# Optimization experiments

Measured on AMD Instinct MI355X. Metric: run time of the kernel, lower is better.

## Reference

```python
import jax, jax.numpy as jnp
import numpy as np

N, E = 65536, 524288
IN_DIM, HID_DIM, OUT_DIM = 1024, 512, 256


def setup_inputs() -> dict:
    key = jax.random.key(0)
    k1, k2, k3, k4, k5, k6 = jax.random.split(key, 6)
    h = jax.random.normal(k1, (N, IN_DIM), dtype=jnp.float32)
    src = jax.random.randint(k2, (E,), 0, N, dtype=jnp.int64)
    dst = jax.random.randint(k3, (E,), 0, N, dtype=jnp.int64)
    # Glorot-uniform weights as in DGL GraphConv
    lim1 = float(np.sqrt(6.0 / (IN_DIM + HID_DIM)))
    lim2 = float(np.sqrt(6.0 / (HID_DIM + OUT_DIM)))
    W1 = jax.random.uniform(k4, (IN_DIM, HID_DIM), jnp.float32, -lim1, lim1)
    W2 = jax.random.uniform(k5, (HID_DIM, OUT_DIM), jnp.float32, -lim2, lim2)
    b1 = jnp.zeros((HID_DIM,), jnp.float32)
    b2 = jnp.zeros((OUT_DIM,), jnp.float32)
    return {"h": h, "W1": W1, "b1": b1, "W2": W2, "b2": b2, "src": src, "dst": dst}


def _graph_conv(x, W, b, src, dst, inv_sqrt_dout, inv_sqrt_din):
    # DGL GraphConv, norm='both': D_in^{-1/2} A D_out^{-1/2} X W + b
    # Apply dense transform first (in_dim >= out_dim path in DGL) -- same math.
    x = x * inv_sqrt_dout[:, None]
    x = x @ W  # [N, out]
    agg = jax.ops.segment_sum(x[src], dst, num_segments=x.shape[0])  # scatter-add over edges
    return agg * inv_sqrt_din[:, None] + b


def reference(h, W1, b1, W2, b2, src, dst):
    n = h.shape[0]
    ones = jnp.ones((src.shape[0],), h.dtype)
    deg_out = jnp.maximum(jax.ops.segment_sum(ones, src, num_segments=n), 1.0)
    deg_in = jnp.maximum(jax.ops.segment_sum(ones, dst, num_segments=n), 1.0)
    inv_sqrt_dout = jax.lax.rsqrt(deg_out)
    inv_sqrt_din = jax.lax.rsqrt(deg_in)
    x = _graph_conv(h, W1, b1, src, dst, inv_sqrt_dout, inv_sqrt_din)
    x = jax.nn.elu(x)  # act; dropout p=0 -> identity
    out = _graph_conv(x, W2, b2, src, dst, inv_sqrt_dout, inv_sqrt_din)
    return out  # last_act = Identity
```

## Files before the change

### kernel.cpp

```cpp
#include <hip/hip_runtime.h>
#include <hip/hip_bf16.h>

#define IN_DIM 1024
#define HID 512
#define OUTD 256

typedef __attribute__((ext_vector_type(8))) short short8;
typedef __attribute__((ext_vector_type(4))) float f32x4;
typedef __attribute__((ext_vector_type(8))) unsigned short ushort8e;
typedef __attribute__((ext_vector_type(4))) unsigned short ushort4e;
typedef __attribute__((ext_vector_type(4))) unsigned int uint4e;

template<int F> struct VecSel;
template<> struct VecSel<8> { using T = ushort8e; };
template<> struct VecSel<4> { using T = ushort4e; };


__device__ inline unsigned short f2bf(float f) {
    union { float f; unsigned u; } v; v.f = f;
    unsigned r = (v.u + 0x7FFF + ((v.u >> 16) & 1)) >> 16;
    return (unsigned short)r;
}

__device__ inline float bf2f(unsigned short u) {
    union { unsigned u; float f; } v; v.u = ((unsigned)u) << 16; return v.f;
}

__device__ inline unsigned pkbf(float a, float b) {
    __hip_bfloat162 h = __float22bfloat162_rn(float2{a, b});
    union { __hip_bfloat162 h; unsigned u; } v; v.h = h; return v.u;
}

__device__ inline void gload16(const void* g, void* l) {
    __builtin_amdgcn_global_load_lds(
        (const __attribute__((address_space(1))) void*)g,
        (__attribute__((address_space(3))) void*)l, 16, 0, 0);
}


__global__ void deg_kernel(const int* __restrict__ src, const int* __restrict__ dst,
                           int* __restrict__ dego, int* __restrict__ degi, int E) {
    int i = blockIdx.x * blockDim.x + threadIdx.x;
    if (i < E) {
        atomicAdd(&dego[src[i]], 1);
        atomicAdd(&degi[dst[i]], 1);
    }
}

__global__ void invsqrt_kernel(const int* __restrict__ dego, const int* __restrict__ degi,
                               float* __restrict__ iso, float* __restrict__ isi, int n) {
    int i = blockIdx.x * blockDim.x + threadIdx.x;
    if (i < n) {
        iso[i] = rsqrtf(fmaxf((float)dego[i], 1.0f));
        isi[i] = rsqrtf(fmaxf((float)degi[i], 1.0f));
    }
}


__global__ __launch_bounds__(256) void scan_block(const int* __restrict__ deg,
                                                  int* __restrict__ excl,
                                                  int* __restrict__ partials) {
    __shared__ int tmp[256];
    int tid = threadIdx.x;
    int i = blockIdx.x * 256 + tid;
    int v = deg[i];
    tmp[tid] = v;
    __syncthreads();
    #pragma unroll
    for (int off = 1; off < 256; off <<= 1) {
        int t = (tid >= off) ? tmp[tid - off] : 0;
        __syncthreads();
        tmp[tid] += t;
        __syncthreads();
    }
    excl[i] = tmp[tid] - v;
    if (tid == 255) partials[blockIdx.x] = tmp[255];
}

__global__ __launch_bounds__(256) void scan_partials(int* __restrict__ partials) {
    __shared__ int tmp[256];
    int tid = threadIdx.x;
    int v = partials[tid];
    tmp[tid] = v;
    __syncthreads();
    #pragma unroll
    for (int off = 1; off < 256; off <<= 1) {
        int t = (tid >= off) ? tmp[tid - off] : 0;
        __syncthreads();
        tmp[tid] += t;
        __syncthreads();
    }
    partials[tid] = tmp[tid] - v;
}

__global__ __launch_bounds__(256) void scan_add(const int* __restrict__ excl,
                                                const int* __restrict__ partials,
                                                const int* __restrict__ deg,
                                                int* __restrict__ row_start,
                                                int* __restrict__ cursor, int n) {
    int i = blockIdx.x * 256 + threadIdx.x;
    int v = excl[i] + partials[blockIdx.x];
    row_start[i] = v;
    cursor[i] = v;
    if (i == n - 1) row_start[n] = v + deg[i];
}

__global__ void csr_fill(const int* __restrict__ src, const int* __restrict__ dst,
                         int* __restrict__ cursor, int* __restrict__ eidx, int E) {
    int e = blockIdx.x * blockDim.x + threadIdx.x;
    if (e < E) {
        int pos = atomicAdd(&cursor[dst[e]], 1);
        eidx[pos] = src[e];
    }
}


__global__ void transpose_cvt(const float* __restrict__ W, unsigned short* __restrict__ Wt,
                              int K, int N) {
    int i = blockIdx.x * 256 + threadIdx.x;
    if (i < N * K) {
        int n = i / K, k = i - n * K;
        Wt[i] = f2bf(W[(size_t)k * N + n]);
    }
}


#define TM 128
#define TN 128
#define TK 64
#define NXCD 8

template<int AF32>
__global__ __launch_bounds__(256) void gemm_bf16_mfma(
    const void* __restrict__ Ap, const unsigned short* __restrict__ Bt,
    unsigned short* __restrict__ Cb, int M, int K, int Nc)
{
    __shared__ unsigned short As[2][TM][TK];
    __shared__ unsigned short Bs[2][TN][TK];

    const int tid  = threadIdx.x;
    const int lane = tid & 63;
    const int wave = tid >> 6;
    const int wr = wave >> 1, wc = wave & 1;
    const int lrow = lane & 15;
    const int lkg  = lane >> 4;

    const int nwg = gridDim.x;
    const int per = nwg / NXCD;
    const int lin = blockIdx.x;
    const int newlin = (lin % NXCD) * per + lin / NXCD;
    const int ncb = Nc / TN;
    const int m0 = (newlin / ncb) * TM;
    const int n0 = (newlin % ncb) * TN;

    int srow[4], sq[4];
    #pragma unroll
    for (int i = 0; i < 4; ++i) {
        int s = i * 256 + wave * 64 + lane;
        srow[i] = s >> 3;
        sq[i] = (s & 7) ^ ((s >> 3) & 7);
    }

    char* AsB = (char*)&As[0][0][0];
    char* BsB = (char*)&Bs[0][0][0];

    const float* Af = (const float*)Ap;
    const unsigned short* Ab = (const unsigned short*)Ap;

    auto stageOp = [&](const unsigned short* G, int rc0, int kt, char* opBase, int buf) {
        const int k0 = kt * TK;
        #pragma unroll
        for (int i = 0; i < 4; ++i)
            gload16(G + (size_t)(rc0 + srow[i]) * K + k0 + sq[i] * 8,
                    opBase + buf * 16384 + (i * 256 + wave * 64) * 16);
    };

    const int rA = tid >> 2;
    const int g  = tid & 3;
    const int qp0 = (2 * g) ^ (rA & 7);
    const int qp1 = (2 * g + 1) ^ (rA & 7);
    float4 L[8];
    auto loadA = [&](int kt) {
        const float* p0 = Af + (size_t)(m0 + rA) * K + kt * TK + g * 16;
        const float* p1 = p0 + (size_t)64 * K;
        L[0] = *reinterpret_cast<const float4*>(p0);
        L[1] = *reinterpret_cast<const float4*>(p0 + 4);
        L[2] = *reinterpret_cast<const float4*>(p0 + 8);
        L[3] = *reinterpret_cast<const float4*>(p0 + 12);
        L[4] = *reinterpret_cast<const float4*>(p1);
        L[5] = *reinterpret_cast<const float4*>(p1 + 4);
        L[6] = *reinterpret_cast<const float4*>(p1 + 8);
        L[7] = *reinterpret_cast<const float4*>(p1 + 12);
    };
    auto writeA = [&](int buf) {
        #pragma unroll
        for (int r = 0; r < 2; ++r) {
            const float4 f0 = L[r * 4 + 0], f1 = L[r * 4 + 1];
            const float4 f2 = L[r * 4 + 2], f3 = L[r * 4 + 3];
            uint4e a, b;
            a[0] = pkbf(f0.x, f0.y); a[1] = pkbf(f0.z, f0.w);
            a[2] = pkbf(f1.x, f1.y); a[3] = pkbf(f1.z, f1.w);
            b[0] = pkbf(f2.x, f2.y); b[1] = pkbf(f2.z, f2.w);
            b[2] = pkbf(f3.x, f3.y); b[3] = pkbf(f3.z, f3.w);
            char* rowb = AsB + buf * 16384 + (rA + r * 64) * 128;
            *reinterpret_cast<uint4e*>(rowb + qp0 * 16) = a;
            *reinterpret_cast<uint4e*>(rowb + qp1 * 16) = b;
        }
    };

    f32x4 acc[4][4] = {};

    stageOp(Bt, n0, 0, BsB, 0);
    if (AF32) { loadA(0); writeA(0); }
    else       stageOp(Ab, m0, 0, AsB, 0);
    __syncthreads();

    const int nk = K / TK;
    for (int kt = 0; kt < nk; ++kt) {
        const int cur = kt & 1, nxt = cur ^ 1;

        if (kt + 1 < nk) {
            stageOp(Bt, n0, kt + 1, BsB, nxt);
            if (AF32) loadA(kt + 1);
            else      stageOp(Ab, m0, kt + 1, AsB, nxt);
        }

        #pragma unroll
        for (int ks = 0; ks < 2; ++ks) {
            short8 af[4], bfr[4];
            #pragma unroll
            for (int mi = 0; mi < 4; ++mi) {
                const int row = wr * 64 + mi * 16 + lrow;
                const int qp = (ks * 4 + lkg) ^ (lrow & 7);
                af[mi] = *reinterpret_cast<const short8*>(&As[cur][row][qp * 8]);
            }
            #pragma unroll
            for (int ni = 0; ni < 4; ++ni) {
                const int row = wc * 64 + ni * 16 + lrow;
                const int qp = (ks * 4 + lkg) ^ (lrow & 7);
                bfr[ni] = *reinterpret_cast<const short8*>(&Bs[cur][row][qp * 8]);
            }
            #pragma unroll
            for (int mi = 0; mi < 4; ++mi)
                #pragma unroll
                for (int ni = 0; ni < 4; ++ni)
                    acc[mi][ni] = __builtin_amdgcn_mfma_f32_16x16x32_bf16(
                        af[mi], bfr[ni], acc[mi][ni], 0, 0, 0);
        }

        if (AF32 && kt + 1 < nk) writeA(nxt);

        __syncthreads();
    }

    #pragma unroll
    for (int mi = 0; mi < 4; ++mi)
        #pragma unroll
        for (int ni = 0; ni < 4; ++ni)
            #pragma unroll
            for (int r = 0; r < 4; ++r)
                Cb[(size_t)(m0 + wr * 64 + mi * 16 + lkg * 4 + r) * Nc
                   + (n0 + wc * 64 + ni * 16 + lrow)] = f2bf(acc[mi][ni][r]);
}


template<int DIM, bool LAYER1>
__global__ __launch_bounds__(256) void aggregate(
    const int* __restrict__ row_start, const int* __restrict__ eidx,
    const unsigned short* __restrict__ Xb, const float* __restrict__ isi,
    const float* __restrict__ iso, const float* __restrict__ bias,
    unsigned short* __restrict__ out_bf, float* __restrict__ out_f)
{
    constexpr int F = DIM / 64;
    using VecT = typename VecSel<F>::T;
    const int node = blockIdx.x * 4 + (threadIdx.x >> 6);
    const int lane = threadIdx.x & 63;

    const int beg = row_start[node];
    const int end = row_start[node + 1];
    const unsigned short* base = Xb + lane * F;

    float acc[F] = {};
    int e = beg;
    for (; e + 3 < end; e += 4) {
        int i0 = eidx[e], i1 = eidx[e + 1], i2 = eidx[e + 2], i3 = eidx[e + 3];
        float s0 = 1.f, s1 = 1.f, s2 = 1.f, s3 = 1.f;
        if (LAYER1) { s0 = iso[i0]; s1 = iso[i1]; s2 = iso[i2]; s3 = iso[i3]; }
        VecT v0 = *reinterpret_cast<const VecT*>(base + (size_t)i0 * DIM);
        VecT v1 = *reinterpret_cast<const VecT*>(base + (size_t)i1 * DIM);
        VecT v2 = *reinterpret_cast<const VecT*>(base + (size_t)i2 * DIM);
        VecT v3 = *reinterpret_cast<const VecT*>(base + (size_t)i3 * DIM);
        #pragma unroll
        for (int f = 0; f < F; ++f) {
            if (LAYER1) {
                acc[f] = fmaf(s0, bf2f(v0[f]), acc[f]);
                acc[f] = fmaf(s1, bf2f(v1[f]), acc[f]);
                acc[f] = fmaf(s2, bf2f(v2[f]), acc[f]);
                acc[f] = fmaf(s3, bf2f(v3[f]), acc[f]);
            } else {
                acc[f] += bf2f(v0[f]); acc[f] += bf2f(v1[f]);
                acc[f] += bf2f(v2[f]); acc[f] += bf2f(v3[f]);
            }
        }
    }
    for (; e < end; ++e) {
        int i0 = eidx[e];
        float s0 = LAYER1 ? iso[i0] : 1.f;
        VecT v0 = *reinterpret_cast<const VecT*>(base + (size_t)i0 * DIM);
        #pragma unroll
        for (int f = 0; f < F; ++f)
            acc[f] = LAYER1 ? fmaf(s0, bf2f(v0[f]), acc[f]) : acc[f] + bf2f(v0[f]);
    }

    const float si = isi[node];
    float bv[F];
    #pragma unroll
    for (int q = 0; q < F / 4; ++q)
        *reinterpret_cast<float4*>(&bv[q * 4]) =
            *reinterpret_cast<const float4*>(bias + lane * F + q * 4);

    if (LAYER1) {
        const float so = iso[node];
        short8 o;
        #pragma unroll
        for (int f = 0; f < F; ++f) {
            float v = acc[f] * si + bv[f];
            v = v > 0.f ? v : expm1f(v);
            o[f] = (short)f2bf(v * so);
        }
        *reinterpret_cast<short8*>(out_bf + (size_t)node * DIM + lane * F) = o;
    } else {
        #pragma unroll
        for (int q = 0; q < F / 4; ++q) {
            float4 v = make_float4(acc[q * 4 + 0] * si + bv[q * 4 + 0],
                                   acc[q * 4 + 1] * si + bv[q * 4 + 1],
                                   acc[q * 4 + 2] * si + bv[q * 4 + 2],
                                   acc[q * 4 + 3] * si + bv[q * 4 + 3]);
            *reinterpret_cast<float4*>(out_f + (size_t)node * DIM + lane * F + q * 4) = v;
        }
    }
}


extern "C" void kernel_launch(void* const* d_in, const int* in_sizes, int n_in,
                              void* d_out, int out_size, void* d_ws, size_t ws_size,
                              hipStream_t stream) {
    const float* h  = (const float*)d_in[0];
    const float* W1 = (const float*)d_in[1];
    const float* b1 = (const float*)d_in[2];
    const float* W2 = (const float*)d_in[3];
    const float* b2 = (const float*)d_in[4];
    const int*   src = (const int*)d_in[5];
    const int*   dst = (const int*)d_in[6];

    const int N = in_sizes[0] / IN_DIM;
    const int E = in_sizes[5];
    float* out = (float*)d_out;

    int* dego      = (int*)d_ws;
    int* degi      = dego + N;
    int* excl      = degi + N;
    int* partials  = excl + N;
    int* row_start = partials + 256;
    int* cursor    = row_start + N + 64;
    int* eidx      = cursor + N;
    float* iso     = (float*)(eidx + E);
    float* isi     = iso + N;
    unsigned short* W1t = (unsigned short*)(isi + N);
    unsigned short* W2t = W1t + (size_t)IN_DIM * HID;
    unsigned short* X1b = W2t + (size_t)HID * OUTD;
    unsigned short* X2b = X1b;
    unsigned short* R2h = X1b + (size_t)N * HID;

    hipMemsetAsync(dego, 0, sizeof(int) * (size_t)2 * N, stream);

    deg_kernel<<<(E + 255) / 256, 256, 0, stream>>>(src, dst, dego, degi, E);
    invsqrt_kernel<<<(N + 255) / 256, 256, 0, stream>>>(dego, degi, iso, isi, N);

    scan_block<<<N / 256, 256, 0, stream>>>(degi, excl, partials);
    scan_partials<<<1, 256, 0, stream>>>(partials);
    scan_add<<<N / 256, 256, 0, stream>>>(excl, partials, degi, row_start, cursor, N);
    csr_fill<<<(E + 255) / 256, 256, 0, stream>>>(src, dst, cursor, eidx, E);

    transpose_cvt<<<(IN_DIM * HID + 255) / 256, 256, 0, stream>>>(W1, W1t, IN_DIM, HID);
    transpose_cvt<<<(HID * OUTD + 255) / 256, 256, 0, stream>>>(W2, W2t, HID, OUTD);

    gemm_bf16_mfma<1><<<(N / TM) * (HID / TN), 256, 0, stream>>>(
        h, W1t, X1b, N, IN_DIM, HID);
    aggregate<HID, true><<<N / 4, 256, 0, stream>>>(
        row_start, eidx, X1b, isi, iso, b1, R2h, nullptr);

    gemm_bf16_mfma<0><<<(N / TM) * (OUTD / TN), 256, 0, stream>>>(
        R2h, W2t, X2b, N, HID, OUTD);
    aggregate<OUTD, false><<<N / 4, 256, 0, stream>>>(
        row_start, eidx, X2b, isi, iso, b2, nullptr, out);
}
```

Measured before the change: 431.7 us.

## Use full-width 64x512 GEMM1 tile with fused out-degree row scaling

Replaces the layer-1 GEMM with a kernel where each block computes a 64-row by full 512-column tile, so the fp32 input matrix is read and converted to bf16 only once instead of once per column tile. The out-degree normalization is folded into the A-load conversion, which removes the per-edge iso gather and FMA from the layer-1 aggregation. The new kernel uses a single LDS buffer with two barriers per K step and no prefetch overlap, and its 128 accumulator tiles per wave raise register pressure. Scaling before the bf16 rounding also shifts where rounding error enters.

Result: slower. 462.9 us (+7.2%).

```diff
diff --git a/kernel.cpp b/kernel.cpp
--- a/kernel.cpp
+++ b/kernel.cpp
@@ -9,7 +9,6 @@
 typedef __attribute__((ext_vector_type(4))) float f32x4;
 typedef __attribute__((ext_vector_type(8))) unsigned short ushort8e;
 typedef __attribute__((ext_vector_type(4))) unsigned short ushort4e;
-typedef __attribute__((ext_vector_type(4))) unsigned int uint4e;
 
 template<int F> struct VecSel;
 template<> struct VecSel<8> { using T = ushort8e; };
@@ -24,11 +23,6 @@
 
 __device__ inline float bf2f(unsigned short u) {
     union { unsigned u; float f; } v; v.u = ((unsigned)u) << 16; return v.f;
-}
-
-__device__ inline unsigned pkbf(float a, float b) {
-    __hip_bfloat162 h = __float22bfloat162_rn(float2{a, b});
-    union { __hip_bfloat162 h; unsigned u; } v; v.h = h; return v.u;
 }
 
 __device__ inline void gload16(const void* g, void* l) {
@@ -125,14 +119,96 @@
 }
 
 
+__global__ __launch_bounds__(256) void gemm1_wide(
+    const float* __restrict__ A, const unsigned short* __restrict__ Bt,
+    const float* __restrict__ rowscale, unsigned short* __restrict__ Cb, int M)
+{
+    __shared__ unsigned short As[64][32];
+    __shared__ unsigned short Bs[512][32];
+
+    const int tid  = threadIdx.x;
+    const int lane = tid & 63;
+    const int wave = tid >> 6;
+    const int lrow = lane & 15;
+    const int lkg  = lane >> 4;
+
+    const int m0 = blockIdx.x * 64;
+
+    char* AsB = (char*)&As[0][0];
+    char* BsB = (char*)&Bs[0][0];
+
+    const int rA = tid >> 2;
+    const int g  = tid & 3;
+    const int qpA = g ^ ((rA >> 1) & 3);
+    const float sc = rowscale[m0 + rA];
+
+    const int rslot = (lkg ^ ((lrow >> 1) & 3)) * 8;
+
+    f32x4 acc[4][8] = {};
+
+    const int nk = IN_DIM / 32;
+    for (int kt = 0; kt < nk; ++kt) {
+        const int k0 = kt * 32;
+
+        #pragma unroll
+        for (int i = 0; i < 8; ++i) {
+            const int s = i * 256 + wave * 64 + lane;
+            const int r = s >> 2;
+            const int q = (s & 3) ^ ((s >> 3) & 3);
+            gload16(Bt + (size_t)r * IN_DIM + k0 + q * 8,
+                    BsB + (i * 256 + wave * 64) * 16);
+        }
+
+        {
+            const float* pa = A + (size_t)(m0 + rA) * IN_DIM + k0 + g * 8;
+            float4 x = *reinterpret_cast<const float4*>(pa);
+            float4 y = *reinterpret_cast<const float4*>(pa + 4);
+            short8 kv;
+            kv[0] = (short)f2bf(x.x * sc); kv[1] = (short)f2bf(x.y * sc);
+            kv[2] = (short)f2bf(x.z * sc); kv[3] = (short)f2bf(x.w * sc);
+            kv[4] = (short)f2bf(y.x * sc); kv[5] = (short)f2bf(y.y * sc);
+            kv[6] = (short)f2bf(y.z * sc); kv[7] = (short)f2bf(y.w * sc);
+            *reinterpret_cast<short8*>(AsB + rA * 64 + qpA * 16) = kv;
+        }
+
+        __syncthreads();
+
+        short8 af[4], bfr[8];
+        #pragma unroll
+        for (int mi = 0; mi < 4; ++mi)
+            af[mi] = *reinterpret_cast<const short8*>(&As[mi * 16 + lrow][rslot]);
+        #pragma unroll
+        for (int ni = 0; ni < 8; ++ni)
+            bfr[ni] = *reinterpret_cast<const short8*>(&Bs[wave * 128 + ni * 16 + lrow][rslot]);
+
+        #pragma unroll
+        for (int mi = 0; mi < 4; ++mi)
+            #pragma unroll
+            for (int ni = 0; ni < 8; ++ni)
+                acc[mi][ni] = __builtin_amdgcn_mfma_f32_16x16x32_bf16(
+                    af[mi], bfr[ni], acc[mi][ni], 0, 0, 0);
+
+        __syncthreads();
+    }
+
+    #pragma unroll
+    for (int mi = 0; mi < 4; ++mi)
+        #pragma unroll
+        for (int ni = 0; ni < 8; ++ni)
+            #pragma unroll
+            for (int r = 0; r < 4; ++r)
+                Cb[(size_t)(m0 + mi * 16 + lkg * 4 + r) * HID
+                   + (wave * 128 + ni * 16 + lrow)] = f2bf(acc[mi][ni][r]);
+}
+
+
 #define TM 128
 #define TN 128
 #define TK 64
 #define NXCD 8
 
-template<int AF32>
-__global__ __launch_bounds__(256) void gemm_bf16_mfma(
-    const void* __restrict__ Ap, const unsigned short* __restrict__ Bt,
+__global__ __launch_bounds__(256) void gemm2_bf16(
+    const unsigned short* __restrict__ Ab, const unsigned short* __restrict__ Bt,
     unsigned short* __restrict__ Cb, int M, int K, int Nc)
 {
     __shared__ unsigned short As[2][TM][TK];
@@ -164,9 +240,6 @@
     char* AsB = (char*)&As[0][0][0];
     char* BsB = (char*)&Bs[0][0][0];
 
-    const float* Af = (const float*)Ap;
-    const unsigned short* Ab = (const unsigned short*)Ap;
-
     auto stageOp = [&](const unsigned short* G, int rc0, int kt, char* opBase, int buf) {
         const int k0 = kt * TK;
         #pragma unroll
@@ -175,44 +248,10 @@
                     opBase + buf * 16384 + (i * 256 + wave * 64) * 16);
     };
 
-    const int rA = tid >> 2;
-    const int g  = tid & 3;
-    const int qp0 = (2 * g) ^ (rA & 7);
-    const int qp1 = (2 * g + 1) ^ (rA & 7);
-    float4 L[8];
-    auto loadA = [&](int kt) {
-        const float* p0 = Af + (size_t)(m0 + rA) * K + kt * TK + g * 16;
-        const float* p1 = p0 + (size_t)64 * K;
-        L[0] = *reinterpret_cast<const float4*>(p0);
-        L[1] = *reinterpret_cast<const float4*>(p0 + 4);
-        L[2] = *reinterpret_cast<const float4*>(p0 + 8);
-        L[3] = *reinterpret_cast<const float4*>(p0 + 12);
-        L[4] = *reinterpret_cast<const float4*>(p1);
-        L[5] = *reinterpret_cast<const float4*>(p1 + 4);
-        L[6] = *reinterpret_cast<const float4*>(p1 + 8);
-        L[7] = *reinterpret_cast<const float4*>(p1 + 12);
-    };
-    auto writeA = [&](int buf) {
-        #pragma unroll
-        for (int r = 0; r < 2; ++r) {
-            const float4 f0 = L[r * 4 + 0], f1 = L[r * 4 + 1];
-            const float4 f2 = L[r * 4 + 2], f3 = L[r * 4 + 3];
-            uint4e a, b;
-            a[0] = pkbf(f0.x, f0.y); a[1] = pkbf(f0.z, f0.w);
-            a[2] = pkbf(f1.x, f1.y); a[3] = pkbf(f1.z, f1.w);
-            b[0] = pkbf(f2.x, f2.y); b[1] = pkbf(f2.z, f2.w);
-            b[2] = pkbf(f3.x, f3.y); b[3] = pkbf(f3.z, f3.w);
-            char* rowb = AsB + buf * 16384 + (rA + r * 64) * 128;
-            *reinterpret_cast<uint4e*>(rowb + qp0 * 16) = a;
-            *reinterpret_cast<uint4e*>(rowb + qp1 * 16) = b;
-        }
-    };
-
     f32x4 acc[4][4] = {};
 
     stageOp(Bt, n0, 0, BsB, 0);
-    if (AF32) { loadA(0); writeA(0); }
-    else       stageOp(Ab, m0, 0, AsB, 0);
+    stageOp(Ab, m0, 0, AsB, 0);
     __syncthreads();
 
     const int nk = K / TK;
@@ -221,8 +260,7 @@
 
         if (kt + 1 < nk) {
             stageOp(Bt, n0, kt + 1, BsB, nxt);
-            if (AF32) loadA(kt + 1);
-            else      stageOp(Ab, m0, kt + 1, AsB, nxt);
+            stageOp(Ab, m0, kt + 1, AsB, nxt);
         }
 
         #pragma unroll
@@ -247,8 +285,6 @@
                     acc[mi][ni] = __builtin_amdgcn_mfma_f32_16x16x32_bf16(
                         af[mi], bfr[ni], acc[mi][ni], 0, 0, 0);
         }
-
-        if (AF32 && kt + 1 < nk) writeA(nxt);
 
         __syncthreads();
     }
@@ -284,32 +320,20 @@
     int e = beg;
     for (; e + 3 < end; e += 4) {
         int i0 = eidx[e], i1 = eidx[e + 1], i2 = eidx[e + 2], i3 = eidx[e + 3];
-        float s0 = 1.f, s1 = 1.f, s2 = 1.f, s3 = 1.f;
-        if (LAYER1) { s0 = iso[i0]; s1 = iso[i1]; s2 = iso[i2]; s3 = iso[i3]; }
         VecT v0 = *reinterpret_cast<const VecT*>(base + (size_t)i0 * DIM);
         VecT v1 = *reinterpret_cast<const VecT*>(base + (size_t)i1 * DIM);
         VecT v2 = *reinterpret_cast<const VecT*>(base + (size_t)i2 * DIM);
         VecT v3 = *reinterpret_cast<const VecT*>(base + (size_t)i3 * DIM);
         #pragma unroll
         for (int f = 0; f < F; ++f) {
-            if (LAYER1) {
-                acc[f] = fmaf(s0, bf2f(v0[f]), acc[f]);
-                acc[f] = fmaf(s1, bf2f(v1[f]), acc[f]);
-                acc[f] = fmaf(s2, bf2f(v2[f]), acc[f]);
-                acc[f] = fmaf(s3, bf2f(v3[f]), acc[f]);
-            } else {
-                acc[f] += bf2f(v0[f]); acc[f] += bf2f(v1[f]);
-                acc[f] += bf2f(v2[f]); acc[f] += bf2f(v3[f]);
-            }
+            acc[f] += bf2f(v0[f]); acc[f] += bf2f(v1[f]);
+            acc[f] += bf2f(v2[f]); acc[f] += bf2f(v3[f]);
         }
     }
     for (; e < end; ++e) {
-        int i0 = eidx[e];
-        float s0 = LAYER1 ? iso[i0] : 1.f;
-        VecT v0 = *reinterpret_cast<const VecT*>(base + (size_t)i0 * DIM);
-        #pragma unroll
-        for (int f = 0; f < F; ++f)
-            acc[f] = LAYER1 ? fmaf(s0, bf2f(v0[f]), acc[f]) : acc[f] + bf2f(v0[f]);
+        VecT v0 = *reinterpret_cast<const VecT*>(base + (size_t)eidx[e] * DIM);
+        #pragma unroll
+        for (int f = 0; f < F; ++f) acc[f] += bf2f(v0[f]);
     }
 
     const float si = isi[node];
@@ -385,12 +409,11 @@
     transpose_cvt<<<(IN_DIM * HID + 255) / 256, 256, 0, stream>>>(W1, W1t, IN_DIM, HID);
     transpose_cvt<<<(HID * OUTD + 255) / 256, 256, 0, stream>>>(W2, W2t, HID, OUTD);
 
-    gemm_bf16_mfma<1><<<(N / TM) * (HID / TN), 256, 0, stream>>>(
-        h, W1t, X1b, N, IN_DIM, HID);
+    gemm1_wide<<<N / 64, 256, 0, stream>>>(h, W1t, iso, X1b, N);
     aggregate<HID, true><<<N / 4, 256, 0, stream>>>(
         row_start, eidx, X1b, isi, iso, b1, R2h, nullptr);
 
-    gemm_bf16_mfma<0><<<(N / TM) * (OUTD / TN), 256, 0, stream>>>(
+    gemm2_bf16<<<(N / TM) * (OUTD / TN), 256, 0, stream>>>(
         R2h, W2t, X2b, N, HID, OUTD);
     aggregate<OUTD, false><<<N / 4, 256, 0, stream>>>(
         row_start, eidx, X2b, isi, iso, b2, nullptr, out);
```
